# Performance work log

Hardware: AMD Instinct MI355X
Metric: run time of the kernel (lower is better)

## Reference

```python
import jax, jax.numpy as jnp
import numpy as np

B, C, H, W = 8, 256, 128, 128
EPS = 1e-12  # F.normalize eps


def setup_inputs() -> dict:
    key = jax.random.key(0)
    k0, k1, k2, k3 = jax.random.split(key, 4)
    x = jax.random.normal(k0, (B, C, H, W), jnp.float32)
    # qkv: Conv2d(C, 3C, 1, bias=False) -> weight [3C, C]
    w_qkv = jax.random.normal(k1, (3 * C, C), jnp.float32) * 0.02
    # qkv_dwconv: Conv2d(3C, 3C, 1, groups=3C) -> per-channel scale [3C]
    w_dw = jax.random.normal(k2, (3 * C,), jnp.float32) * 0.1 + 1.0
    # temperature: Parameter(ones(num_heads=1, 1, 1))
    temperature = jnp.ones((1, 1, 1), jnp.float32)
    # project_out: Conv2d(C, C, 1, bias=False) -> weight [C, C]
    w_proj = jax.random.normal(k3, (C, C), jnp.float32) * 0.02
    return {"x": x, "w_qkv": w_qkv, "w_dw": w_dw,
            "temperature": temperature, "w_proj": w_proj}


def reference(x, w_qkv, w_dw, temperature, w_proj):
    b, c, h, w = x.shape
    n = h * w
    # pointwise conv + depthwise 1x1 conv (= per-channel scale)
    qkv = jnp.einsum('bchw,oc->bohw', x, w_qkv) * w_dw[None, :, None, None]
    q, k, v = jnp.split(qkv, 3, axis=1)          # each [b, c, h, w]
    q = q.reshape(b, c, n)
    k = k.reshape(b, c, n)
    v = v.reshape(b, c, n)
    # L2-normalize along spatial dim (F.normalize: x / max(||x||, eps))
    q = q / jnp.maximum(jnp.linalg.norm(q, axis=-1, keepdims=True), EPS)
    k = k / jnp.maximum(jnp.linalg.norm(k, axis=-1, keepdims=True), EPS)
    # channel-wise cosine attention: [b, c, c]
    attn = jnp.einsum('bcn,bdn->bcd', q, k) * temperature[0]
    attn = jax.nn.softmax(attn, axis=-1)
    out = jnp.einsum('bcd,bdn->bcn', attn, v).reshape(b, c, h, w)
    out = jnp.einsum('bchw,oc->bohw', out, w_proj)
    return out
```

## Files before the change

### kernel.cpp

```cpp
#include <hip/hip_runtime.h>
#include <hip/hip_bf16.h>
#include <stdint.h>

#define NB 8
#define NC 256
#define NN 16384
#define KS 64

typedef short bf16x8 __attribute__((ext_vector_type(8)));
typedef float f32x4  __attribute__((ext_vector_type(4)));
typedef uint32_t u32;

__device__ __forceinline__ unsigned short f2bf(float f) {
  union { float f; unsigned u; } c; c.f = f;
  return (unsigned short)((c.u + 0x7FFFu + ((c.u >> 16) & 1u)) >> 16);
}
__device__ __forceinline__ float bf2f(unsigned short h) {
  union { unsigned u; float f; } c; c.u = ((unsigned)h) << 16;
  return c.f;
}

__device__ __forceinline__ bf16x8 pack8(float4 lo, float4 hi) {
  union { bf16x8 v; __hip_bfloat162 h[4]; } u;
  u.h[0] = __float22bfloat162_rn(make_float2(lo.x, lo.y));
  u.h[1] = __float22bfloat162_rn(make_float2(lo.z, lo.w));
  u.h[2] = __float22bfloat162_rn(make_float2(hi.x, hi.y));
  u.h[3] = __float22bfloat162_rn(make_float2(hi.z, hi.w));
  return u.v;
}

__device__ __forceinline__ void gload16(const void* g, void* l) {
  __builtin_amdgcn_global_load_lds(
      (const __attribute__((address_space(1))) u32*)g,
      (__attribute__((address_space(3))) u32*)l, 16, 0, 0);
}

__device__ __forceinline__ void stage_tile(const char* src, int ld_bytes,
                                           char* lds, int w, int l) {
#pragma unroll
  for (int i = 0; i < 4; ++i) {
    int s = (w * 4 + i) * 64 + l;
    int row = s >> 3;
    int srcslot = (l & 7) ^ (row & 7);
    gload16(src + (size_t)row * ld_bytes + srcslot * 16,
            lds + (w * 4 + i) * 1024);
  }
}

__device__ __forceinline__ void gemm_core(const char* A, int lda_b,
                                          const char* Bm, int ldb_b, int ktiles,
                                          char* smem, int tid, f32x4 acc[4][4]) {
  const int w = tid >> 6, l = tid & 63;
  const int wm = w >> 1, wn = w & 1;
  char* As = smem;
  char* Bs = smem + 16384;
  for (int kt = 0; kt < ktiles; ++kt) {
    stage_tile(A + kt * 128, lda_b, As, w, l);
    stage_tile(Bm + kt * 128, ldb_b, Bs, w, l);
    __syncthreads();
#pragma unroll
    for (int ks = 0; ks < 2; ++ks) {
      bf16x8 av[4], bv[4];
      const int kb = ks * 64 + ((l >> 4) << 4);
#pragma unroll
      for (int m = 0; m < 4; ++m) {
        int row = wm * 64 + m * 16 + (l & 15);
        av[m] = *(const bf16x8*)(As + row * 128 + (kb ^ ((row & 7) << 4)));
      }
#pragma unroll
      for (int nq = 0; nq < 4; ++nq) {
        int row = wn * 64 + nq * 16 + (l & 15);
        bv[nq] = *(const bf16x8*)(Bs + row * 128 + (kb ^ ((row & 7) << 4)));
      }
#pragma unroll
      for (int m = 0; m < 4; ++m)
#pragma unroll
        for (int nq = 0; nq < 4; ++nq)
          acc[m][nq] = __builtin_amdgcn_mfma_f32_16x16x32_bf16(
              av[m], bv[nq], acc[m][nq], 0, 0, 0);
    }
    __syncthreads();
  }
}

__global__ __launch_bounds__(256) void k_prepw2(const float* __restrict__ wqkv,
                                                const float* __restrict__ wdw,
                                                float* __restrict__ Wcat,
                                                float* __restrict__ WkT,
                                                float* __restrict__ Wv2) {
  const int r = blockIdx.x, t = threadIdx.x;
  Wcat[r * 256 + t] = wqkv[r * 256 + t] * wdw[r];
  float kv = wqkv[(256 + r) * 256 + t] * wdw[256 + r];
  Wcat[65536 + r * 256 + t] = kv;
  WkT[t * 256 + r] = kv;
  Wv2[r * 256 + t] = wqkv[(512 + r) * 256 + t] * wdw[512 + r];
}

__global__ __launch_bounds__(512, 2) void k_gramT(const float* __restrict__ x,
                                                  unsigned short* __restrict__ gpart,
                                                  char* __restrict__ xt) {
  __shared__ __align__(16) float tile[256 * 64];
  const int tid = threadIdx.x;
  const int ks = blockIdx.x, b = blockIdx.y;
  const int w = tid >> 6, l = tid & 63;
  const int wm = w >> 2, wn = w & 3;
  f32x4 acc[8][4];
#pragma unroll
  for (int m = 0; m < 8; ++m)
#pragma unroll
    for (int n = 0; n < 4; ++n) acc[m][n] = (f32x4){0.f, 0.f, 0.f, 0.f};
  const float* x0 = x + (size_t)b * NC * NN + (size_t)ks * 256;

  for (int kt = 0; kt < 4; ++kt) {
#pragma unroll
    for (int i = 0; i < 8; ++i) {
      int c = (w * 8 + i) * 64 + l;
      int row = c >> 4, slot = c & 15;
      int sl = slot ^ (row & 15);
      gload16(x0 + (size_t)row * NN + kt * 64 + sl * 4,
              (char*)tile + (w * 8 + i) * 1024);
    }
    __syncthreads();
#pragma unroll
    for (int ks2 = 0; ks2 < 2; ++ks2) {
      const int s0 = ks2 * 8 + (l >> 4) * 2;
      bf16x8 av[8], bv[4];
#pragma unroll
      for (int m = 0; m < 8; ++m) {
        int row = wm * 128 + m * 16 + (l & 15);
        float4 lo = *(const float4*)&tile[row * 64 + ((s0 ^ (row & 15)) * 4)];
        float4 hi = *(const float4*)&tile[row * 64 + (((s0 + 1) ^ (row & 15)) * 4)];
        av[m] = pack8(lo, hi);
      }
#pragma unroll
      for (int n = 0; n < 4; ++n) {
        int row = wn * 64 + n * 16 + (l & 15);
        float4 lo = *(const float4*)&tile[row * 64 + ((s0 ^ (row & 15)) * 4)];
        float4 hi = *(const float4*)&tile[row * 64 + (((s0 + 1) ^ (row & 15)) * 4)];
        bv[n] = pack8(lo, hi);
      }
#pragma unroll
      for (int m = 0; m < 8; ++m)
#pragma unroll
        for (int n = 0; n < 4; ++n)
          acc[m][n] = __builtin_amdgcn_mfma_f32_16x16x32_bf16(
              av[m], bv[n], acc[m][n], 0, 0, 0);
    }
    {
      const int n4 = tid >> 5, c8 = tid & 31;
      const int gn = ks * 256 + kt * 64 + n4 * 4;
      float vr[8][4];
#pragma unroll
      for (int j = 0; j < 8; ++j) {
        int c = c8 * 8 + j;
        float4 v = *(const float4*)&tile[c * 64 + ((n4 ^ (c & 15)) * 4)];
        vr[j][0] = v.x; vr[j][1] = v.y; vr[j][2] = v.z; vr[j][3] = v.w;
      }
#pragma unroll
      for (int k = 0; k < 4; ++k) {
        unsigned short ov[8] __attribute__((aligned(16)));
#pragma unroll
        for (int j = 0; j < 8; ++j) ov[j] = f2bf(vr[j][k]);
        *(uint4*)(xt + (((size_t)b * NN + gn + k) * 256 + c8 * 8) * 2) =
            *(const uint4*)(ov);
      }
    }
    __syncthreads();
  }
  unsigned short* gp = gpart + ((size_t)(ks * NB + b)) * 65536;
#pragma unroll
  for (int m = 0; m < 8; ++m)
#pragma unroll
    for (int n = 0; n < 4; ++n)
#pragma unroll
      for (int r = 0; r < 4; ++r) {
        int c = wm * 128 + m * 16 + ((l >> 4) << 2) + r;
        int d = wn * 64 + n * 16 + (l & 15);
        gp[(size_t)c * 256 + d] = f2bf(acc[m][n][r]);
      }
}

__global__ __launch_bounds__(256) void k_reduceG(
    const unsigned short* __restrict__ gpart, float* __restrict__ G) {
  const int t = threadIdx.x;
  const int c = blockIdx.x * 2 + (t >> 7), b = blockIdx.y;
  const int d0 = (t & 127) * 2;
  float s0 = 0.f, s1 = 0.f;
#pragma unroll 8
  for (int ks = 0; ks < KS; ++ks) {
    u32 v = *(const u32*)(gpart + (((size_t)ks * NB + b) * 256 + c) * 256 + d0);
    s0 += bf2f((unsigned short)(v & 0xffff));
    s1 += bf2f((unsigned short)(v >> 16));
  }
  *(float2*)(G + ((size_t)b * 256 + c) * 256 + d0) = make_float2(s0, s1);
}

__global__ __launch_bounds__(256) void k_sgT(const float* __restrict__ Wcat,
                                             const float* __restrict__ G,
                                             float* __restrict__ T12,
                                             float* __restrict__ nqk) {
  const int t = threadIdx.x;
  const int r0 = blockIdx.x * 8, b = blockIdx.y;
  const float* Gb = G + (size_t)b * 65536 + t;
  float acc[8] = {0, 0, 0, 0, 0, 0, 0, 0};
#pragma unroll 4
  for (int k = 0; k < 256; ++k) {
    float bv = Gb[(size_t)k * 256];
#pragma unroll
    for (int o = 0; o < 8; ++o) acc[o] += Wcat[(r0 + o) * 256 + k] * bv;
  }
#pragma unroll
  for (int o = 0; o < 8; ++o)
    T12[(size_t)b * 131072 + (size_t)(r0 + o) * 256 + t] = acc[o];
  __shared__ float red[8][4];
  const int w = t >> 6, l = t & 63;
#pragma unroll
  for (int o = 0; o < 8; ++o) {
    float s = acc[o] * Wcat[(r0 + o) * 256 + t];
#pragma unroll
    for (int off = 32; off; off >>= 1) s += __shfl_xor(s, off);
    if (l == 0) red[o][w] = s;
  }
  __syncthreads();
  if (t < 8)
    nqk[b * 512 + r0 + t] = red[t][0] + red[t][1] + red[t][2] + red[t][3];
}

__global__ __launch_bounds__(256) void k_ssoft(const float* __restrict__ T12,
                                               const float* __restrict__ WkT,
                                               const float* __restrict__ nqk,
                                               const float* __restrict__ temp,
                                               float* __restrict__ attn) {
  const int t = threadIdx.x;
  const int c0 = blockIdx.x * 8, b = blockIdx.y;
  const float* Ab = T12 + (size_t)b * 131072 + (size_t)c0 * 256;
  const float* Bb = WkT + t;
  float acc[8] = {0, 0, 0, 0, 0, 0, 0, 0};
#pragma unroll 4
  for (int k = 0; k < 256; ++k) {
    float bv = Bb[(size_t)k * 256];
#pragma unroll
    for (int o = 0; o < 8; ++o) acc[o] += Ab[o * 256 + k] * bv;
  }
  const float rk = 1.0f / fmaxf(sqrtf(fmaxf(nqk[b * 512 + 256 + t], 0.f)), 1e-12f);
  const float tau = temp[0];
#pragma unroll
  for (int o = 0; o < 8; ++o) {
    float rq = 1.0f / fmaxf(sqrtf(fmaxf(nqk[b * 512 + c0 + o], 0.f)), 1e-12f);
    acc[o] = acc[o] * rq * rk * tau;
  }
  __shared__ float redm[8][4];
  __shared__ float reds[8][4];
  const int w = t >> 6, l = t & 63;
#pragma unroll
  for (int o = 0; o < 8; ++o) {
    float m = acc[o];
#pragma unroll
    for (int off = 32; off; off >>= 1) m = fmaxf(m, __shfl_xor(m, off));
    if (l == 0) redm[o][w] = m;
  }
  __syncthreads();
  float e[8];
#pragma unroll
  for (int o = 0; o < 8; ++o) {
    float m = fmaxf(fmaxf(redm[o][0], redm[o][1]), fmaxf(redm[o][2], redm[o][3]));
    e[o] = __expf(acc[o] - m);
    float s = e[o];
#pragma unroll
    for (int off = 32; off; off >>= 1) s += __shfl_xor(s, off);
    if (l == 0) reds[o][w] = s;
  }
  __syncthreads();
#pragma unroll
  for (int o = 0; o < 8; ++o) {
    float tot = reds[o][0] + reds[o][1] + reds[o][2] + reds[o][3];
    attn[(size_t)b * 65536 + (size_t)(c0 + o) * 256 + t] = e[o] / tot;
  }
}

__global__ __launch_bounds__(256) void k_sg2x(const float* __restrict__ wp,
                                              const float* __restrict__ attn,
                                              const float* __restrict__ wv2,
                                              char* __restrict__ Fb) {
  __shared__ float P[8 * 256];
  const int t = threadIdx.x;
  const int o0 = blockIdx.x * 8, b = blockIdx.y;
  const float* Ab = wp + (size_t)o0 * 256;
  const float* Bb = attn + (size_t)b * 65536 + t;
  float acc[8] = {0, 0, 0, 0, 0, 0, 0, 0};
#pragma unroll 4
  for (int k = 0; k < 256; ++k) {
    float bv = Bb[(size_t)k * 256];
#pragma unroll
    for (int o = 0; o < 8; ++o) acc[o] += Ab[o * 256 + k] * bv;
  }
#pragma unroll
  for (int o = 0; o < 8; ++o) P[o * 256 + t] = acc[o];
  __syncthreads();
  float a2[8] = {0, 0, 0, 0, 0, 0, 0, 0};
  const float* Bv = wv2 + t;
#pragma unroll 4
  for (int k = 0; k < 256; ++k) {
    float bv = Bv[(size_t)k * 256];
#pragma unroll
    for (int o = 0; o < 8; ++o) a2[o] += P[o * 256 + k] * bv;
  }
  unsigned short* Cp = (unsigned short*)Fb + (size_t)b * 65536;
#pragma unroll
  for (int o = 0; o < 8; ++o) Cp[(size_t)(o0 + o) * 256 + t] = f2bf(a2[o]);
}

__global__ __launch_bounds__(256) void k_final(const char* __restrict__ xt,
                                               const char* __restrict__ fb,
                                               float* __restrict__ out) {
  __shared__ char smem[65536];
  const int tid = threadIdx.x;
  const int nt = blockIdx.x, ot = blockIdx.y, b = blockIdx.z;
  f32x4 acc[4][4];
#pragma unroll
  for (int m = 0; m < 4; ++m)
#pragma unroll
    for (int nq = 0; nq < 4; ++nq) acc[m][nq] = (f32x4){0.f, 0.f, 0.f, 0.f};
  const char* Ap = xt + ((size_t)b * NN + (size_t)nt * 128) * 512;
  const char* Bp = fb + ((size_t)(b * 256 + ot * 128)) * 512;
  gemm_core(Ap, 512, Bp, 512, 4, smem, tid, acc);
  const int w = tid >> 6, l = tid & 63, wm = w >> 1, wn = w & 1;
#pragma unroll
  for (int m = 0; m < 4; ++m)
#pragma unroll
    for (int nq = 0; nq < 4; ++nq)
#pragma unroll
      for (int r = 0; r < 4; ++r) {
        int i = wm * 64 + m * 16 + ((l >> 4) << 2) + r;
        int j = wn * 64 + nq * 16 + (l & 15);
        *(float*)(smem + j * 512 + ((i * 4) ^ ((j & 7) << 4))) = acc[m][nq][r];
      }
  __syncthreads();
  const int j = tid >> 1, h = tid & 1;
  float* dst = out + ((size_t)(b * 256 + ot * 128 + j)) * NN + nt * 128;
#pragma unroll
  for (int cc = 0; cc < 16; ++cc) {
    int ch = h * 16 + cc;
    *(uint4*)(dst + ch * 4) =
        *(const uint4*)(smem + j * 512 + ((ch * 16) ^ ((j & 7) << 4)));
  }
}

extern "C" void kernel_launch(void* const* d_in, const int* in_sizes, int n_in,
                              void* d_out, int out_size, void* d_ws, size_t ws_size,
                              hipStream_t stream) {
  const float* x     = (const float*)d_in[0];
  const float* wqkv  = (const float*)d_in[1];
  const float* wdwf  = (const float*)d_in[2];
  const float* temp  = (const float*)d_in[3];
  const float* wproj = (const float*)d_in[4];
  float* out = (float*)d_out;
  char* ws = (char*)d_ws;

  char*  xt    = ws;
  unsigned short* gpart = (unsigned short*)(ws + 67108864);
  float* G     = (float*)(ws + 134217728);
  float* T12   = (float*)(ws + 136314880);
  float* attn  = (float*)(ws + 140509184);
  char*  Fb    = ws + 142606336;
  float* Wcat  = (float*)(ws + 143654912);
  float* WkT   = (float*)(ws + 144179200);
  float* Wv2   = (float*)(ws + 144441344);
  float* nqk   = (float*)(ws + 144703488);

  k_prepw2<<<dim3(256), dim3(256), 0, stream>>>(wqkv, wdwf, Wcat, WkT, Wv2);
  k_gramT<<<dim3(KS, NB), dim3(512), 0, stream>>>(x, gpart, xt);
  k_reduceG<<<dim3(128, NB), dim3(256), 0, stream>>>(gpart, G);
  k_sgT<<<dim3(64, NB), dim3(256), 0, stream>>>(Wcat, G, T12, nqk);
  k_ssoft<<<dim3(32, NB), dim3(256), 0, stream>>>(T12, WkT, nqk, temp, attn);
  k_sg2x<<<dim3(32, NB), dim3(256), 0, stream>>>(wproj, attn, Wv2, Fb);
  k_final<<<dim3(128, 2, NB), dim3(256), 0, stream>>>(xt, Fb, out);
}
```

Before: 247.0 us.

## Fold weight prep into gram kernel and double-buffer final GEMM loads

After: 246.4 us. About the same (-0.2%).

```diff
diff --git a/kernel.cpp b/kernel.cpp
--- a/kernel.cpp
+++ b/kernel.cpp
@@ -47,61 +47,28 @@
   }
 }
 
-__device__ __forceinline__ void gemm_core(const char* A, int lda_b,
-                                          const char* Bm, int ldb_b, int ktiles,
-                                          char* smem, int tid, f32x4 acc[4][4]) {
-  const int w = tid >> 6, l = tid & 63;
-  const int wm = w >> 1, wn = w & 1;
-  char* As = smem;
-  char* Bs = smem + 16384;
-  for (int kt = 0; kt < ktiles; ++kt) {
-    stage_tile(A + kt * 128, lda_b, As, w, l);
-    stage_tile(Bm + kt * 128, ldb_b, Bs, w, l);
-    __syncthreads();
-#pragma unroll
-    for (int ks = 0; ks < 2; ++ks) {
-      bf16x8 av[4], bv[4];
-      const int kb = ks * 64 + ((l >> 4) << 4);
-#pragma unroll
-      for (int m = 0; m < 4; ++m) {
-        int row = wm * 64 + m * 16 + (l & 15);
-        av[m] = *(const bf16x8*)(As + row * 128 + (kb ^ ((row & 7) << 4)));
-      }
-#pragma unroll
-      for (int nq = 0; nq < 4; ++nq) {
-        int row = wn * 64 + nq * 16 + (l & 15);
-        bv[nq] = *(const bf16x8*)(Bs + row * 128 + (kb ^ ((row & 7) << 4)));
-      }
-#pragma unroll
-      for (int m = 0; m < 4; ++m)
-#pragma unroll
-        for (int nq = 0; nq < 4; ++nq)
-          acc[m][nq] = __builtin_amdgcn_mfma_f32_16x16x32_bf16(
-              av[m], bv[nq], acc[m][nq], 0, 0, 0);
-    }
-    __syncthreads();
-  }
-}
-
-__global__ __launch_bounds__(256) void k_prepw2(const float* __restrict__ wqkv,
-                                                const float* __restrict__ wdw,
-                                                float* __restrict__ Wcat,
-                                                float* __restrict__ WkT,
-                                                float* __restrict__ Wv2) {
-  const int r = blockIdx.x, t = threadIdx.x;
-  Wcat[r * 256 + t] = wqkv[r * 256 + t] * wdw[r];
-  float kv = wqkv[(256 + r) * 256 + t] * wdw[256 + r];
-  Wcat[65536 + r * 256 + t] = kv;
-  WkT[t * 256 + r] = kv;
-  Wv2[r * 256 + t] = wqkv[(512 + r) * 256 + t] * wdw[512 + r];
-}
-
-__global__ __launch_bounds__(512, 2) void k_gramT(const float* __restrict__ x,
-                                                  unsigned short* __restrict__ gpart,
-                                                  char* __restrict__ xt) {
+__global__ __launch_bounds__(512, 2) void k_gramT(
+    const float* __restrict__ x, unsigned short* __restrict__ gpart,
+    char* __restrict__ xt,
+    const float* __restrict__ wqkv, const float* __restrict__ wdw,
+    float* __restrict__ Wcat, float* __restrict__ WkT,
+    float* __restrict__ Wv2) {
   __shared__ __align__(16) float tile[256 * 64];
+  const int bid = blockIdx.x;
   const int tid = threadIdx.x;
-  const int ks = blockIdx.x, b = blockIdx.y;
+
+  if (bid >= KS * NB) {
+    const int r = (bid - KS * NB) * 2 + (tid >> 8);
+    const int t = tid & 255;
+    Wcat[r * 256 + t] = wqkv[r * 256 + t] * wdw[r];
+    float kv = wqkv[(256 + r) * 256 + t] * wdw[256 + r];
+    Wcat[65536 + r * 256 + t] = kv;
+    WkT[t * 256 + r] = kv;
+    Wv2[r * 256 + t] = wqkv[(512 + r) * 256 + t] * wdw[512 + r];
+    return;
+  }
+
+  const int ks = bid & (KS - 1), b = bid >> 6;
   const int w = tid >> 6, l = tid & 63;
   const int wm = w >> 2, wn = w & 3;
   f32x4 acc[8][4];
@@ -316,6 +283,8 @@
   __shared__ char smem[65536];
   const int tid = threadIdx.x;
   const int nt = blockIdx.x, ot = blockIdx.y, b = blockIdx.z;
+  const int w = tid >> 6, l = tid & 63;
+  const int wm = w >> 1, wn = w & 1;
   f32x4 acc[4][4];
 #pragma unroll
   for (int m = 0; m < 4; ++m)
@@ -323,8 +292,41 @@
     for (int nq = 0; nq < 4; ++nq) acc[m][nq] = (f32x4){0.f, 0.f, 0.f, 0.f};
   const char* Ap = xt + ((size_t)b * NN + (size_t)nt * 128) * 512;
   const char* Bp = fb + ((size_t)(b * 256 + ot * 128)) * 512;
-  gemm_core(Ap, 512, Bp, 512, 4, smem, tid, acc);
-  const int w = tid >> 6, l = tid & 63, wm = w >> 1, wn = w & 1;
+
+  stage_tile(Ap, 512, smem, w, l);
+  stage_tile(Bp, 512, smem + 16384, w, l);
+  __syncthreads();
+  for (int kt = 0; kt < 4; ++kt) {
+    if (kt < 3) {
+      char* nb = smem + ((kt + 1) & 1) * 32768;
+      stage_tile(Ap + (kt + 1) * 128, 512, nb, w, l);
+      stage_tile(Bp + (kt + 1) * 128, 512, nb + 16384, w, l);
+    }
+    const char* As = smem + (kt & 1) * 32768;
+    const char* Bs = As + 16384;
+#pragma unroll
+    for (int ks = 0; ks < 2; ++ks) {
+      bf16x8 av[4], bv[4];
+      const int kb = ks * 64 + ((l >> 4) << 4);
+#pragma unroll
+      for (int m = 0; m < 4; ++m) {
+        int row = wm * 64 + m * 16 + (l & 15);
+        av[m] = *(const bf16x8*)(As + row * 128 + (kb ^ ((row & 7) << 4)));
+      }
+#pragma unroll
+      for (int nq = 0; nq < 4; ++nq) {
+        int row = wn * 64 + nq * 16 + (l & 15);
+        bv[nq] = *(const bf16x8*)(Bs + row * 128 + (kb ^ ((row & 7) << 4)));
+      }
+#pragma unroll
+      for (int m = 0; m < 4; ++m)
+#pragma unroll
+        for (int nq = 0; nq < 4; ++nq)
+          acc[m][nq] = __builtin_amdgcn_mfma_f32_16x16x32_bf16(
+              av[m], bv[nq], acc[m][nq], 0, 0, 0);
+    }
+    __syncthreads();
+  }
 #pragma unroll
   for (int m = 0; m < 4; ++m)
 #pragma unroll
@@ -368,8 +370,8 @@
   float* Wv2   = (float*)(ws + 144441344);
   float* nqk   = (float*)(ws + 144703488);
 
-  k_prepw2<<<dim3(256), dim3(256), 0, stream>>>(wqkv, wdwf, Wcat, WkT, Wv2);
-  k_gramT<<<dim3(KS, NB), dim3(512), 0, stream>>>(x, gpart, xt);
+  k_gramT<<<dim3(KS * NB + 128), dim3(512), 0, stream>>>(
+      x, gpart, xt, wqkv, wdwf, Wcat, WkT, Wv2);
   k_reduceG<<<dim3(128, NB), dim3(256), 0, stream>>>(gpart, G);
   k_sgT<<<dim3(64, NB), dim3(256), 0, stream>>>(Wcat, G, T12, nqk);
   k_ssoft<<<dim3(32, NB), dim3(256), 0, stream>>>(T12, WkT, nqk, temp, attn);
```
